# Optimization experiments

Hardware: AMD Instinct MI355X
Metric: run time of the kernel (lower is better)

## Reference

```python
import jax, jax.numpy as jnp
import numpy as np

N_LAYERS = 8
LAYER_NAMES = ['self', 'cross'] * 4
D_MODEL = 256
NHEAD = 8
HEAD_DIM = D_MODEL // NHEAD
EPS_ATTN = 1e-6
EPS_LN = 1e-5


def _xavier(key, shape):
    fan_in, fan_out = shape[-2], shape[-1]
    limit = float(np.sqrt(6.0 / (fan_in + fan_out)))
    return jax.random.uniform(key, shape, jnp.float32, -limit, limit)


def setup_inputs() -> dict:
    key = jax.random.key(0)
    ks = jax.random.split(key, 9)
    B, L, C = 4, 4800, D_MODEL
    inp = {
        'feat0': jax.random.normal(ks[0], (B, L, C), jnp.float32),
        'feat1': jax.random.normal(ks[1], (B, L, C), jnp.float32),
        # stacked per-layer params (layers are deepcopies, independently init'd)
        'Wq': _xavier(ks[2], (N_LAYERS, C, C)),
        'Wk': _xavier(ks[3], (N_LAYERS, C, C)),
        'Wv': _xavier(ks[4], (N_LAYERS, C, C)),
        'Wm': _xavier(ks[5], (N_LAYERS, C, C)),
        'W1': _xavier(ks[6], (N_LAYERS, 2 * C, 2 * C)),
        'W2': _xavier(ks[7], (N_LAYERS, 2 * C, C)),
        'ln1_w': jnp.ones((N_LAYERS, C), jnp.float32),
        'ln1_b': jnp.zeros((N_LAYERS, C), jnp.float32),
        'ln2_w': jnp.ones((N_LAYERS, C), jnp.float32),
        'ln2_b': jnp.zeros((N_LAYERS, C), jnp.float32),
    }
    return inp


def _layernorm(x, w, b):
    mu = jnp.mean(x, axis=-1, keepdims=True)
    var = jnp.mean(jnp.square(x - mu), axis=-1, keepdims=True)
    return (x - mu) * jax.lax.rsqrt(var + EPS_LN) * w + b


def _encoder_layer(x, source, Wq, Wk, Wv, Wm, W1, W2, ln1_w, ln1_b, ln2_w, ln2_b):
    bs, L, C = x.shape
    S = source.shape[1]
    q = (x @ Wq).reshape(bs, L, NHEAD, HEAD_DIM)
    k = (source @ Wk).reshape(bs, S, NHEAD, HEAD_DIM)
    v = (source @ Wv).reshape(bs, S, NHEAD, HEAD_DIM)
    # linear (kernelized) attention: phi(x) = elu(x) + 1
    Q = jax.nn.elu(q) + 1.0
    K = jax.nn.elu(k) + 1.0
    v_len = S
    v_scaled = v / v_len
    KV = jnp.einsum('nshd,nshv->nhdv', K, v_scaled)          # [N,H,D,D]
    Z = 1.0 / (jnp.einsum('nlhd,nhd->nlh', Q, K.sum(axis=1)) + EPS_ATTN)
    msg = jnp.einsum('nlhd,nhdv,nlh->nlhv', Q, KV, Z) * v_len  # [N,L,H,D]
    msg = msg.reshape(bs, L, C) @ Wm
    msg = _layernorm(msg, ln1_w, ln1_b)
    h = jnp.concatenate([x, msg], axis=-1)                   # [N,L,2C]
    h = jnp.maximum(h @ W1, 0.0) @ W2
    h = _layernorm(h, ln2_w, ln2_b)
    return x + h


def reference(feat0, feat1, Wq, Wk, Wv, Wm, W1, W2, ln1_w, ln1_b, ln2_w, ln2_b):
    for i, name in enumerate(LAYER_NAMES):
        p = (Wq[i], Wk[i], Wv[i], Wm[i], W1[i], W2[i],
             ln1_w[i], ln1_b[i], ln2_w[i], ln2_b[i])
        if name == 'self':
            feat0 = _encoder_layer(feat0, feat0, *p)
            feat1 = _encoder_layer(feat1, feat1, *p)
        else:  # cross
            feat0 = _encoder_layer(feat0, feat1, *p)
            feat1 = _encoder_layer(feat1, feat0, *p)
    return (feat0, feat1)
```

## Files before the change

kernel.cpp:

```cpp
#include <hip/hip_runtime.h>

typedef __attribute__((ext_vector_type(8))) short short8;
typedef __attribute__((ext_vector_type(4))) float f32x4;

#define DEV static __device__ __forceinline__

DEV unsigned short f2bf(float x) {
  union { float f; unsigned int u; } c; c.f = x;
  unsigned int r = c.u + 0x7fffu + ((c.u >> 16) & 1u);
  return (unsigned short)(r >> 16);
}
DEV float bf2f(unsigned short s) {
  union { unsigned int u; float f; } c; c.u = ((unsigned int)s) << 16;
  return c.f;
}
DEV float elu1(float x) { return x > 0.f ? x + 1.f : __expf(x); }

DEV void gload_lds16(const void* g, void* l) {
  __builtin_amdgcn_global_load_lds(
      (const __attribute__((address_space(1))) unsigned int*)g,
      (__attribute__((address_space(3))) unsigned int*)l, 16, 0, 0);
}

__global__ __launch_bounds__(256)
void wprep(const float* __restrict__ src, unsigned short* __restrict__ dst,
           int K, int N, int dls) {
  const int layer = blockIdx.z;
  src += (size_t)layer * K * N;
  dst += (size_t)layer * dls;
  __shared__ float tile[64][65];
  const int n0 = blockIdx.x * 64, k0 = blockIdx.y * 64;
  const int c = threadIdx.x & 63, r4 = threadIdx.x >> 6;
#pragma unroll
  for (int i = 0; i < 16; ++i) {
    int r = (i << 2) + r4;
    tile[r][c] = src[(size_t)(k0 + r) * N + n0 + c];
  }
  __syncthreads();
#pragma unroll
  for (int i = 0; i < 16; ++i) {
    int r = (i << 2) + r4;
    dst[(size_t)(n0 + r) * K + k0 + c] = f2bf(tile[c][r]);
  }
}

__global__ __launch_bounds__(256)
void init_feat(const float* __restrict__ src, float* __restrict__ dstf,
               unsigned short* __restrict__ dstb, int n4) {
  int i = blockIdx.x * 256 + threadIdx.x;
  if (i >= n4) return;
  float4 v = ((const float4*)src)[i];
  ((float4*)dstf)[i] = v;
  ushort4 o;
  o.x = f2bf(v.x); o.y = f2bf(v.y); o.z = f2bf(v.z); o.w = f2bf(v.w);
  ((ushort4*)dstb)[i] = o;
}

template<int EPI>
__global__ __launch_bounds__(256)
void gemm_bt(const unsigned short* __restrict__ A0,
             const unsigned short* __restrict__ A1,
             const unsigned short* __restrict__ BT,
             unsigned short* __restrict__ Cb, unsigned short* __restrict__ Cb2,
             int M, int N, int K, int lda) {
  __shared__ __align__(16) unsigned short smem[16896];
  unsigned short* As = smem;
  unsigned short* Bs = smem + 8192;
  const int tid = threadIdx.x;
  const int lane = tid & 63, wave = tid >> 6;
  const int tn = N >> 7;
  const int bm = (int)blockIdx.x / tn, bn = (int)blockIdx.x % tn;
  const int wm = (wave >> 1) << 6, wn = (wave & 1) << 6;
  const int lr = lane & 15, lk = lane >> 4;

  f32x4 acc[4][4];
#pragma unroll
  for (int i = 0; i < 4; ++i)
#pragma unroll
    for (int j = 0; j < 4; ++j) acc[i][j] = (f32x4){0.f, 0.f, 0.f, 0.f};

  for (int k0 = 0; k0 < K; k0 += 64) {
#pragma unroll
    for (int i = 0; i < 4; ++i) {
      const int cb = (i << 2) + wave;
      const int id = (cb << 6) + lane;
      const int row = id >> 3, ck = id & 7;
      const int gk = k0 + ((ck ^ (row & 7)) << 3);
      const unsigned short* srcA;
      if (A1) {
        srcA = (gk < 256) ? (A0 + (size_t)(bm * 128 + row) * 256 + gk)
                          : (A1 + (size_t)(bm * 128 + row) * 256 + (gk - 256));
      } else {
        srcA = A0 + (size_t)(bm * 128 + row) * lda + gk;
      }
      gload_lds16(srcA, As + (size_t)cb * 512);
      const unsigned short* srcB = BT + (size_t)(bn * 128 + row) * K + gk;
      gload_lds16(srcB, Bs + (size_t)cb * 512);
    }
    __syncthreads();
#pragma unroll
    for (int kk = 0; kk < 2; ++kk) {
      short8 af[4], bfr[4];
#pragma unroll
      for (int mi = 0; mi < 4; ++mi) {
        const int row = wm + mi * 16 + lr;
        const int ck = ((kk << 2) + lk) ^ (row & 7);
        af[mi] = *(const short8*)(As + row * 64 + ck * 8);
      }
#pragma unroll
      for (int ni = 0; ni < 4; ++ni) {
        const int row = wn + ni * 16 + lr;
        const int ck = ((kk << 2) + lk) ^ (row & 7);
        bfr[ni] = *(const short8*)(Bs + row * 64 + ck * 8);
      }
#pragma unroll
      for (int mi = 0; mi < 4; ++mi)
#pragma unroll
        for (int ni = 0; ni < 4; ++ni)
          acc[mi][ni] = __builtin_amdgcn_mfma_f32_16x16x32_bf16(af[mi], bfr[ni], acc[mi][ni], 0, 0, 0);
    }
    __syncthreads();
  }

  unsigned short* dst;
  int cstride, colofs, act;
  if (EPI == 1)      { dst = Cb;  cstride = N;   colofs = bn * 128; act = 1; }
  else if (EPI == 2) { dst = Cb;  cstride = 512; colofs = bn * 128; act = (bn < 2) ? 2 : 0; }
  else if (EPI == 3) { dst = Cb;  cstride = 256; colofs = bn * 128; act = 2; }
  else {
    if (bn < 2) { dst = Cb;  cstride = 256; colofs = bn * 128;       act = 2; }
    else        { dst = Cb2; cstride = 512; colofs = bn * 128 - 256; act = (bn < 4) ? 2 : 0; }
  }

  unsigned short* Ct = smem;
  const int cr = lk << 2;
#pragma unroll
  for (int mi = 0; mi < 4; ++mi)
#pragma unroll
    for (int ni = 0; ni < 4; ++ni)
#pragma unroll
      for (int j = 0; j < 4; ++j) {
        float v = acc[mi][ni][j];
        v = (act == 1) ? fmaxf(v, 0.f) : (act == 2) ? elu1(v) : v;
        Ct[(wm + mi * 16 + cr + j) * 132 + (wn + ni * 16 + lr)] = f2bf(v);
      }
  __syncthreads();
  const int rr = lane >> 4, cc8 = (lane & 15) << 3;
#pragma unroll
  for (int s = 0; s < 8; ++s) {
    const int rl = (wave << 5) + (s << 2) + rr;
    uint2 lo = *(const uint2*)(Ct + rl * 132 + cc8);
    uint2 hi = *(const uint2*)(Ct + rl * 132 + cc8 + 4);
    uint4 val = make_uint4(lo.x, lo.y, hi.x, hi.y);
    *(uint4*)(dst + (size_t)(bm * 128 + rl) * cstride + colofs + cc8) = val;
  }
}

template<int EPI>
__global__ __launch_bounds__(512)
void gemm_ln(const unsigned short* __restrict__ A, const unsigned short* __restrict__ BT,
             const float* __restrict__ lnw, const float* __restrict__ lnb,
             const float* __restrict__ xres, float* __restrict__ outf,
             unsigned short* __restrict__ outb, int K) {
  __shared__ __align__(16) unsigned short smem[24576];
  unsigned short* As = smem;
  unsigned short* Bs = smem + 8192;
  const int tid = threadIdx.x;
  const int lane = tid & 63, wid = tid >> 6;
  const int bm = blockIdx.x;
  const int wm = (wid >> 2) << 6, wn = (wid & 3) << 6;
  const int lr = lane & 15, lk = lane >> 4;

  f32x4 acc[4][4];
#pragma unroll
  for (int i = 0; i < 4; ++i)
#pragma unroll
    for (int j = 0; j < 4; ++j) acc[i][j] = (f32x4){0.f, 0.f, 0.f, 0.f};

  for (int k0 = 0; k0 < K; k0 += 64) {
#pragma unroll
    for (int i = 0; i < 2; ++i) {
      const int cb = i * 8 + wid;
      const int id = (cb << 6) + lane;
      const int row = id >> 3, ck = id & 7;
      const int gk = k0 + ((ck ^ (row & 7)) << 3);
      gload_lds16(A + (size_t)(bm * 128 + row) * K + gk, As + (size_t)cb * 512);
    }
#pragma unroll
    for (int i = 0; i < 4; ++i) {
      const int cb = i * 8 + wid;
      const int id = (cb << 6) + lane;
      const int row = id >> 3, ck = id & 7;
      const int gk = k0 + ((ck ^ (row & 7)) << 3);
      gload_lds16(BT + (size_t)row * K + gk, Bs + (size_t)cb * 512);
    }
    __syncthreads();
#pragma unroll
    for (int kk = 0; kk < 2; ++kk) {
      short8 af[4], bfr[4];
#pragma unroll
      for (int mi = 0; mi < 4; ++mi) {
        const int row = wm + mi * 16 + lr;
        const int ck = ((kk << 2) + lk) ^ (row & 7);
        af[mi] = *(const short8*)(As + row * 64 + ck * 8);
      }
#pragma unroll
      for (int ni = 0; ni < 4; ++ni) {
        const int row = wn + ni * 16 + lr;
        const int ck = ((kk << 2) + lk) ^ (row & 7);
        bfr[ni] = *(const short8*)(Bs + row * 64 + ck * 8);
      }
#pragma unroll
      for (int mi = 0; mi < 4; ++mi)
#pragma unroll
        for (int ni = 0; ni < 4; ++ni)
          acc[mi][ni] = __builtin_amdgcn_mfma_f32_16x16x32_bf16(af[mi], bfr[ni], acc[mi][ni], 0, 0, 0);
    }
    __syncthreads();
  }

  float* red = (float*)smem;
  const int cr = lk << 2;
  float wv[4], bv[4];
#pragma unroll
  for (int ni = 0; ni < 4; ++ni) {
    wv[ni] = lnw[wn + ni * 16 + lr];
    bv[ni] = lnb[wn + ni * 16 + lr];
  }
#pragma unroll
  for (int mi = 0; mi < 4; ++mi) {
#pragma unroll
    for (int j = 0; j < 4; ++j) {
      float s = 0.f, q = 0.f;
#pragma unroll
      for (int ni = 0; ni < 4; ++ni) {
        float v = acc[mi][ni][j];
        s += v; q += v * v;
      }
#pragma unroll
      for (int o = 1; o < 16; o <<= 1) {
        s += __shfl_xor(s, o);
        q += __shfl_xor(q, o);
      }
      if (lr == 0) {
        int row = wm + mi * 16 + cr + j;
        red[row * 8 + (wid & 3) * 2] = s;
        red[row * 8 + (wid & 3) * 2 + 1] = q;
      }
    }
  }
  __syncthreads();

  unsigned short* Pt = smem + 2048;
#pragma unroll
  for (int th = 0; th < 2; ++th) {
    if ((wm >> 6) == th) {
#pragma unroll
      for (int mi = 0; mi < 4; ++mi) {
#pragma unroll
        for (int j = 0; j < 4; ++j) {
          const int lrow = mi * 16 + cr + j;
          const int row = wm + lrow;
          const size_t grow = (size_t)bm * 128 + row;
          float s = red[row * 8] + red[row * 8 + 2] + red[row * 8 + 4] + red[row * 8 + 6];
          float q = red[row * 8 + 1] + red[row * 8 + 3] + red[row * 8 + 5] + red[row * 8 + 7];
          float mu = s * (1.f / 256.f);
          float var = q * (1.f / 256.f) - mu * mu;
          float rstd = rsqrtf(var + 1e-5f);
#pragma unroll
          for (int ni = 0; ni < 4; ++ni) {
            int col = wn + ni * 16 + lr;
            float y = (acc[mi][ni][j] - mu) * rstd * wv[ni] + bv[ni];
            if (EPI == 0) {
              Pt[lrow * 264 + col] = f2bf(y);
            } else {
              float o = xres[grow * 256 + col] + y;
              outf[grow * 256 + col] = o;
              Pt[lrow * 264 + col] = f2bf(o);
            }
          }
        }
      }
    }
    __syncthreads();
#pragma unroll
    for (int s = 0; s < 4; ++s) {
      const int qid = wid * 256 + lane * 4 + s;
      const int row = qid >> 5, colq = (qid & 31) << 3;
      uint2 lo = *(const uint2*)(Pt + row * 264 + colq);
      uint2 hi = *(const uint2*)(Pt + row * 264 + colq + 4);
      uint4 val = make_uint4(lo.x, lo.y, hi.x, hi.y);
      *(uint4*)(outb + (size_t)(bm * 128 + th * 64 + row) * 256 + colq) = val;
    }
    __syncthreads();
  }
}

__global__ __launch_bounds__(256)
void kv_partial(const unsigned short* __restrict__ kvb, float* __restrict__ part) {
  const int ch = blockIdx.x, h = blockIdx.y, n = blockIdx.z;
  const int t = threadIdx.x, wave = t >> 6, lane = t & 63;
  __shared__ float kb[4][8][36];
  __shared__ float vb[4][8][36];
  const int dq = lane >> 3, vq = lane & 7;
  float a[4][4];
  float ks[4] = {0.f, 0.f, 0.f, 0.f};
#pragma unroll
  for (int i = 0; i < 4; ++i)
#pragma unroll
    for (int j = 0; j < 4; ++j) a[i][j] = 0.f;

  const int s_base = ch * 480 + wave * 120;
  const int half = lane >> 5, l = lane & 31, r = l >> 2, c8 = l & 3;
  const unsigned short* src = kvb + ((size_t)n * 4800 + s_base + r) * 512 +
                              half * 256 + h * 32 + c8 * 8;
  float* dst = (half ? &vb[wave][r][0] : &kb[wave][r][0]) + c8 * 8;

  for (int it = 0; it < 15; ++it) {
    __syncthreads();
    short8 raw = *(const short8*)(src + (size_t)it * 8 * 512);
#pragma unroll
    for (int e = 0; e < 8; ++e) dst[e] = bf2f((unsigned short)raw[e]);
    __syncthreads();
#pragma unroll
    for (int si = 0; si < 8; ++si) {
      float4 kq = *(const float4*)&kb[wave][si][dq * 4];
      float4 vv = *(const float4*)&vb[wave][si][vq * 4];
      ks[0] += kq.x; ks[1] += kq.y; ks[2] += kq.z; ks[3] += kq.w;
      a[0][0] += kq.x * vv.x; a[0][1] += kq.x * vv.y; a[0][2] += kq.x * vv.z; a[0][3] += kq.x * vv.w;
      a[1][0] += kq.y * vv.x; a[1][1] += kq.y * vv.y; a[1][2] += kq.y * vv.z; a[1][3] += kq.y * vv.w;
      a[2][0] += kq.z * vv.x; a[2][1] += kq.z * vv.y; a[2][2] += kq.z * vv.z; a[2][3] += kq.z * vv.w;
      a[3][0] += kq.w * vv.x; a[3][1] += kq.w * vv.y; a[3][2] += kq.w * vv.z; a[3][3] += kq.w * vv.w;
    }
  }
  float* pb = part + ((size_t)((n * 8 + h) * 40 + ch * 4 + wave)) * 1056;
#pragma unroll
  for (int i = 0; i < 4; ++i) {
#pragma unroll
    for (int j = 0; j < 4; ++j) pb[(dq * 4 + i) * 32 + vq * 4 + j] = a[i][j];
    if (vq == 0) pb[1024 + dq * 4 + i] = ks[i];
  }
}

__global__ __launch_bounds__(256)
void kv_reduce(const float* __restrict__ part, unsigned short* __restrict__ KVb,
               float* __restrict__ Ksum) {
  const int nh = blockIdx.x, t = threadIdx.x;
  const float* pb = part + (size_t)nh * 40 * 1056;
#pragma unroll
  for (int j = 0; j < 4; ++j) {
    int e = t * 4 + j;
    float s = 0.f;
    for (int c = 0; c < 40; ++c) s += pb[c * 1056 + e];
    int dd = e >> 5, vv = e & 31;
    size_t addr = ((size_t)(nh * 2 + (vv >> 4)) * 64 + ((dd >> 3) * 16 + (vv & 15))) * 8 + (dd & 7);
    KVb[addr] = f2bf(s);
  }
  if (t < 32) {
    float s = 0.f;
    for (int c = 0; c < 40; ++c) s += pb[c * 1056 + 1024 + t];
    Ksum[nh * 32 + t] = s;
  }
}

__global__ __launch_bounds__(256)
void msg_kernel(const unsigned short* __restrict__ qb, const unsigned short* __restrict__ KVb,
                const float* __restrict__ Ksum, unsigned short* __restrict__ msg, int qoff) {
  const int n = blockIdx.y;
  const int wave = threadIdx.x >> 6, lane = threadIdx.x & 63;
  const int lr = lane & 15, lk = lane >> 4;
  const int lrow = blockIdx.x * 64 + wave * 16 + lr;
  const unsigned short* qrow = qb + ((size_t)qoff + (size_t)n * 4800 + lrow) * 256;
  const short8* kvv = (const short8*)KVb;
  for (int h = 0; h < 8; ++h) {
    short8 af = *(const short8*)(qrow + h * 32 + lk * 8);
    const float* ksp = Ksum + (n * 8 + h) * 32 + lk * 8;
    float zp = 0.f;
#pragma unroll
    for (int j = 0; j < 8; ++j) zp += bf2f((unsigned short)af[j]) * ksp[j];
    zp += __shfl_xor(zp, 16);
    zp += __shfl_xor(zp, 32);
    float z = 1.f / (zp + 1e-6f);
    short8 b0 = kvv[((size_t)(n * 8 + h) * 2 + 0) * 64 + lane];
    short8 b1 = kvv[((size_t)(n * 8 + h) * 2 + 1) * 64 + lane];
    f32x4 acc0 = (f32x4){0.f, 0.f, 0.f, 0.f}, acc1 = (f32x4){0.f, 0.f, 0.f, 0.f};
    acc0 = __builtin_amdgcn_mfma_f32_16x16x32_bf16(af, b0, acc0, 0, 0, 0);
    acc1 = __builtin_amdgcn_mfma_f32_16x16x32_bf16(af, b1, acc1, 0, 0, 0);
#pragma unroll
    for (int j = 0; j < 4; ++j) {
      int rr = lk * 4 + j;
      float zj = __shfl(z, rr);
      int row = blockIdx.x * 64 + wave * 16 + rr;
      size_t base = ((size_t)n * 4800 + row) * 256 + h * 32;
      msg[base + lr] = f2bf(acc0[j] * zj);
      msg[base + 16 + lr] = f2bf(acc1[j] * zj);
    }
  }
}

extern "C" void kernel_launch(void* const* d_in, const int* in_sizes, int n_in,
                              void* d_out, int out_size, void* d_ws, size_t ws_size,
                              hipStream_t stream) {
  (void)in_sizes; (void)n_in; (void)out_size; (void)ws_size;
  const float* feat0 = (const float*)d_in[0];
  const float* feat1 = (const float*)d_in[1];
  const float* Wq = (const float*)d_in[2];
  const float* Wk = (const float*)d_in[3];
  const float* Wv = (const float*)d_in[4];
  const float* Wm = (const float*)d_in[5];
  const float* W1 = (const float*)d_in[6];
  const float* W2 = (const float*)d_in[7];
  const float* ln1w = (const float*)d_in[8];
  const float* ln1b = (const float*)d_in[9];
  const float* ln2w = (const float*)d_in[10];
  const float* ln2b = (const float*)d_in[11];

  float* F0 = (float*)d_out;
  float* F1 = F0 + (size_t)4915200;

  size_t off = 0;
  auto alloc = [&](size_t bytes) -> void* {
    void* p = (char*)d_ws + off;
    off += (bytes + 255) & ~(size_t)255;
    return p;
  };
  unsigned short* Fb     = (unsigned short*)alloc((size_t)38400 * 256 * 2);
  unsigned short* qb     = (unsigned short*)alloc((size_t)38400 * 256 * 2);
  unsigned short* kvb    = (unsigned short*)alloc((size_t)38400 * 512 * 2);
  unsigned short* msgb   = (unsigned short*)alloc((size_t)38400 * 256 * 2);
  unsigned short* msglnb = (unsigned short*)alloc((size_t)38400 * 256 * 2);
  float*          part   = (float*)alloc((size_t)64 * 40 * 1056 * 4);
  unsigned short* KVb    = (unsigned short*)alloc((size_t)65536 * 2);
  float*          Ksum   = (float*)alloc((size_t)2048 * 4);
  unsigned short* WqkvT  = (unsigned short*)alloc((size_t)8 * 196608 * 2);
  unsigned short* WmT    = (unsigned short*)alloc((size_t)8 * 65536 * 2);
  unsigned short* W1T    = (unsigned short*)alloc((size_t)8 * 262144 * 2);
  unsigned short* W2T    = (unsigned short*)alloc((size_t)8 * 131072 * 2);
  unsigned short* h1b = kvb;
  unsigned short* F0b = Fb;
  unsigned short* F1b = Fb + (size_t)19200 * 256;

  init_feat<<<4800, 256, 0, stream>>>(feat0, F0, F0b, 1228800);
  init_feat<<<4800, 256, 0, stream>>>(feat1, F1, F1b, 1228800);

  wprep<<<dim3(4, 4, 8), 256, 0, stream>>>(Wq, WqkvT, 256, 256, 196608);
  wprep<<<dim3(4, 4, 8), 256, 0, stream>>>(Wk, WqkvT + 65536, 256, 256, 196608);
  wprep<<<dim3(4, 4, 8), 256, 0, stream>>>(Wv, WqkvT + 131072, 256, 256, 196608);
  wprep<<<dim3(4, 4, 8), 256, 0, stream>>>(Wm, WmT, 256, 256, 65536);
  wprep<<<dim3(8, 8, 8), 256, 0, stream>>>(W1, W1T, 512, 512, 262144);
  wprep<<<dim3(4, 8, 8), 256, 0, stream>>>(W2, W2T, 512, 256, 131072);

  auto ffn = [&](unsigned short* Xb, float* X, int M, int i) {
    const int g128 = M >> 7;
    gemm_ln<0><<<g128, 512, 0, stream>>>(msgb, WmT + (size_t)i * 65536,
                                         ln1w + i * 256, ln1b + i * 256,
                                         nullptr, nullptr, msglnb, 256);
    gemm_bt<1><<<g128 * 4, 256, 0, stream>>>(Xb, msglnb, W1T + (size_t)i * 262144,
                                             h1b, nullptr, M, 512, 512, 256);
    gemm_ln<1><<<g128, 512, 0, stream>>>(h1b, W2T + (size_t)i * 131072,
                                         ln2w + i * 256, ln2b + i * 256,
                                         X, X, Xb, 512);
  };

  for (int i = 0; i < 8; ++i) {
    if ((i & 1) == 0) {
      gemm_bt<4><<<1800, 256, 0, stream>>>(Fb, nullptr, WqkvT + (size_t)i * 196608,
                                           qb, kvb, 38400, 768, 256, 256);
      kv_partial<<<dim3(10, 8, 8), 256, 0, stream>>>(kvb, part);
      kv_reduce<<<64, 256, 0, stream>>>(part, KVb, Ksum);
      msg_kernel<<<dim3(75, 8), 256, 0, stream>>>(qb, KVb, Ksum, msgb, 0);
      ffn(Fb, F0, 38400, i);
    } else {
      gemm_bt<3><<<600, 256, 0, stream>>>(Fb, nullptr, WqkvT + (size_t)i * 196608,
                                          qb, nullptr, 38400, 256, 256, 256);
      gemm_bt<2><<<600, 256, 0, stream>>>(F1b, nullptr, WqkvT + (size_t)i * 196608 + 65536,
                                          kvb, nullptr, 19200, 512, 256, 256);
      kv_partial<<<dim3(10, 8, 4), 256, 0, stream>>>(kvb, part);
      kv_reduce<<<32, 256, 0, stream>>>(part, KVb, Ksum);
      msg_kernel<<<dim3(75, 4), 256, 0, stream>>>(qb, KVb, Ksum, msgb, 0);
      ffn(F0b, F0, 19200, i);
      gemm_bt<2><<<600, 256, 0, stream>>>(F0b, nullptr, WqkvT + (size_t)i * 196608 + 65536,
                                          kvb, nullptr, 19200, 512, 256, 256);
      kv_partial<<<dim3(10, 8, 4), 256, 0, stream>>>(kvb, part);
      kv_reduce<<<32, 256, 0, stream>>>(part, KVb, Ksum);
      msg_kernel<<<dim3(75, 4), 256, 0, stream>>>(qb, KVb, Ksum, msgb, 19200);
      ffn(F1b, F1, 19200, i);
    }
  }
}
```

Measured before the change: 1.681 ms.

## Double-buffer LDS tiles in both GEMM kernels to overlap loads with MFMA

Both GEMM kernels now keep two LDS buffers and issue the global-to-LDS loads for the next K tile before computing on the current one. Partial vmcnt waits plus raw barriers replace the full __syncthreads, so that memory latency overlaps with MFMA work. This doubles LDS use per block (64KB and 96KB), which may lower occupancy. The hand-written vmcnt counts must match the number of outstanding loads per thread, or tiles could be read before they arrive.

```diff
diff --git a/kernel.cpp b/kernel.cpp
--- a/kernel.cpp
+++ b/kernel.cpp
@@ -63,9 +63,9 @@
              const unsigned short* __restrict__ BT,
              unsigned short* __restrict__ Cb, unsigned short* __restrict__ Cb2,
              int M, int N, int K, int lda) {
-  __shared__ __align__(16) unsigned short smem[16896];
+  __shared__ __align__(16) unsigned short smem[32768];
   unsigned short* As = smem;
-  unsigned short* Bs = smem + 8192;
+  unsigned short* Bs = smem + 16384;
   const int tid = threadIdx.x;
   const int lane = tid & 63, wave = tid >> 6;
   const int tn = N >> 7;
@@ -79,7 +79,7 @@
 #pragma unroll
     for (int j = 0; j < 4; ++j) acc[i][j] = (f32x4){0.f, 0.f, 0.f, 0.f};
 
-  for (int k0 = 0; k0 < K; k0 += 64) {
+  auto stageAB = [&](int nb, int k0) {
 #pragma unroll
     for (int i = 0; i < 4; ++i) {
       const int cb = (i << 2) + wave;
@@ -93,11 +93,26 @@
       } else {
         srcA = A0 + (size_t)(bm * 128 + row) * lda + gk;
       }
-      gload_lds16(srcA, As + (size_t)cb * 512);
+      gload_lds16(srcA, As + nb * 8192 + (size_t)cb * 512);
       const unsigned short* srcB = BT + (size_t)(bn * 128 + row) * K + gk;
-      gload_lds16(srcB, Bs + (size_t)cb * 512);
-    }
-    __syncthreads();
+      gload_lds16(srcB, Bs + nb * 8192 + (size_t)cb * 512);
+    }
+  };
+
+  const int nt = K >> 6;
+  stageAB(0, 0);
+  for (int t = 0; t < nt; ++t) {
+    const int cur = t & 1;
+    if (t + 1 < nt) {
+      stageAB(cur ^ 1, (t + 1) << 6);
+      asm volatile("s_waitcnt vmcnt(8)" ::: "memory");
+    } else {
+      asm volatile("s_waitcnt vmcnt(0)" ::: "memory");
+    }
+    __builtin_amdgcn_s_barrier();
+    __builtin_amdgcn_sched_barrier(0);
+    const unsigned short* Ac = As + cur * 8192;
+    const unsigned short* Bc = Bs + cur * 8192;
 #pragma unroll
     for (int kk = 0; kk < 2; ++kk) {
       short8 af[4], bfr[4];
@@ -105,13 +120,13 @@
       for (int mi = 0; mi < 4; ++mi) {
         const int row = wm + mi * 16 + lr;
         const int ck = ((kk << 2) + lk) ^ (row & 7);
-        af[mi] = *(const short8*)(As + row * 64 + ck * 8);
+        af[mi] = *(const short8*)(Ac + row * 64 + ck * 8);
       }
 #pragma unroll
       for (int ni = 0; ni < 4; ++ni) {
         const int row = wn + ni * 16 + lr;
         const int ck = ((kk << 2) + lk) ^ (row & 7);
-        bfr[ni] = *(const short8*)(Bs + row * 64 + ck * 8);
+        bfr[ni] = *(const short8*)(Bc + row * 64 + ck * 8);
       }
 #pragma unroll
       for (int mi = 0; mi < 4; ++mi)
@@ -119,7 +134,8 @@
         for (int ni = 0; ni < 4; ++ni)
           acc[mi][ni] = __builtin_amdgcn_mfma_f32_16x16x32_bf16(af[mi], bfr[ni], acc[mi][ni], 0, 0, 0);
     }
-    __syncthreads();
+    __builtin_amdgcn_s_barrier();
+    __builtin_amdgcn_sched_barrier(0);
   }
 
   unsigned short* dst;
@@ -162,9 +178,9 @@
              const float* __restrict__ lnw, const float* __restrict__ lnb,
              const float* __restrict__ xres, float* __restrict__ outf,
              unsigned short* __restrict__ outb, int K) {
-  __shared__ __align__(16) unsigned short smem[24576];
+  __shared__ __align__(16) unsigned short smem[49152];
   unsigned short* As = smem;
-  unsigned short* Bs = smem + 8192;
+  unsigned short* Bs = smem + 16384;
   const int tid = threadIdx.x;
   const int lane = tid & 63, wid = tid >> 6;
   const int bm = blockIdx.x;
@@ -177,14 +193,14 @@
 #pragma unroll
     for (int j = 0; j < 4; ++j) acc[i][j] = (f32x4){0.f, 0.f, 0.f, 0.f};
 
-  for (int k0 = 0; k0 < K; k0 += 64) {
+  auto stageAB = [&](int nb, int k0) {
 #pragma unroll
     for (int i = 0; i < 2; ++i) {
       const int cb = i * 8 + wid;
       const int id = (cb << 6) + lane;
       const int row = id >> 3, ck = id & 7;
       const int gk = k0 + ((ck ^ (row & 7)) << 3);
-      gload_lds16(A + (size_t)(bm * 128 + row) * K + gk, As + (size_t)cb * 512);
+      gload_lds16(A + (size_t)(bm * 128 + row) * K + gk, As + nb * 8192 + (size_t)cb * 512);
     }
 #pragma unroll
     for (int i = 0; i < 4; ++i) {
@@ -192,9 +208,24 @@
       const int id = (cb << 6) + lane;
       const int row = id >> 3, ck = id & 7;
       const int gk = k0 + ((ck ^ (row & 7)) << 3);
-      gload_lds16(BT + (size_t)row * K + gk, Bs + (size_t)cb * 512);
-    }
-    __syncthreads();
+      gload_lds16(BT + (size_t)row * K + gk, Bs + nb * 16384 + (size_t)cb * 512);
+    }
+  };
+
+  const int nt = K >> 6;
+  stageAB(0, 0);
+  for (int t = 0; t < nt; ++t) {
+    const int cur = t & 1;
+    if (t + 1 < nt) {
+      stageAB(cur ^ 1, (t + 1) << 6);
+      asm volatile("s_waitcnt vmcnt(6)" ::: "memory");
+    } else {
+      asm volatile("s_waitcnt vmcnt(0)" ::: "memory");
+    }
+    __builtin_amdgcn_s_barrier();
+    __builtin_amdgcn_sched_barrier(0);
+    const unsigned short* Ac = As + cur * 8192;
+    const unsigned short* Bc = Bs + cur * 16384;
 #pragma unroll
     for (int kk = 0; kk < 2; ++kk) {
       short8 af[4], bfr[4];
@@ -202,13 +233,13 @@
       for (int mi = 0; mi < 4; ++mi) {
         const int row = wm + mi * 16 + lr;
         const int ck = ((kk << 2) + lk) ^ (row & 7);
-        af[mi] = *(const short8*)(As + row * 64 + ck * 8);
+        af[mi] = *(const short8*)(Ac + row * 64 + ck * 8);
       }
 #pragma unroll
       for (int ni = 0; ni < 4; ++ni) {
         const int row = wn + ni * 16 + lr;
         const int ck = ((kk << 2) + lk) ^ (row & 7);
-        bfr[ni] = *(const short8*)(Bs + row * 64 + ck * 8);
+        bfr[ni] = *(const short8*)(Bc + row * 64 + ck * 8);
       }
 #pragma unroll
       for (int mi = 0; mi < 4; ++mi)
@@ -216,7 +247,8 @@
         for (int ni = 0; ni < 4; ++ni)
           acc[mi][ni] = __builtin_amdgcn_mfma_f32_16x16x32_bf16(af[mi], bfr[ni], acc[mi][ni], 0, 0, 0);
     }
-    __syncthreads();
+    __builtin_amdgcn_s_barrier();
+    __builtin_amdgcn_sched_barrier(0);
   }
 
   float* red = (float*)smem;
```

Measured after the change: 1.731 ms. 1.03x slower.

## Restructure kv_partial to load full KV rows via direct global-to-LDS copies

Applied to the files above, without the earlier changes.

kv_partial now assigns each block a chunk of 120 rows across all 8 heads, with each wave handling two heads, instead of one head per block with waves splitting rows. Each step copies whole 8-row slabs of the bf16 K|V buffer into LDS with global_load_lds and converts to float at compute time. This replaces narrow per-head strided global reads and per-element LDS float stores with contiguous row loads. In exchange each thread holds twice the accumulators, and the grid shrinks from 640 to 320 blocks, which lowers parallelism.

```diff
diff --git a/kernel.cpp b/kernel.cpp
--- a/kernel.cpp
+++ b/kernel.cpp
@@ -298,47 +298,60 @@
 
 __global__ __launch_bounds__(256)
 void kv_partial(const unsigned short* __restrict__ kvb, float* __restrict__ part) {
-  const int ch = blockIdx.x, h = blockIdx.y, n = blockIdx.z;
-  const int t = threadIdx.x, wave = t >> 6, lane = t & 63;
-  __shared__ float kb[4][8][36];
-  __shared__ float vb[4][8][36];
+  const int ch = blockIdx.x, n = blockIdx.y;
+  const int tid = threadIdx.x, wid = tid >> 6, lane = tid & 63;
+  __shared__ __align__(16) unsigned short kvs[8 * 512];
   const int dq = lane >> 3, vq = lane & 7;
-  float a[4][4];
-  float ks[4] = {0.f, 0.f, 0.f, 0.f};
-#pragma unroll
-  for (int i = 0; i < 4; ++i)
-#pragma unroll
-    for (int j = 0; j < 4; ++j) a[i][j] = 0.f;
-
-  const int s_base = ch * 480 + wave * 120;
-  const int half = lane >> 5, l = lane & 31, r = l >> 2, c8 = l & 3;
-  const unsigned short* src = kvb + ((size_t)n * 4800 + s_base + r) * 512 +
-                              half * 256 + h * 32 + c8 * 8;
-  float* dst = (half ? &vb[wave][r][0] : &kb[wave][r][0]) + c8 * 8;
+  float a[2][4][4];
+  float ks[2][4];
+#pragma unroll
+  for (int hh = 0; hh < 2; ++hh) {
+#pragma unroll
+    for (int i = 0; i < 4; ++i) {
+      ks[hh][i] = 0.f;
+#pragma unroll
+      for (int j = 0; j < 4; ++j) a[hh][i][j] = 0.f;
+    }
+  }
+  const int r0 = ch * 120;
+  const size_t rowbase = (size_t)n * 4800 + r0;
 
   for (int it = 0; it < 15; ++it) {
     __syncthreads();
-    short8 raw = *(const short8*)(src + (size_t)it * 8 * 512);
-#pragma unroll
-    for (int e = 0; e < 8; ++e) dst[e] = bf2f((unsigned short)raw[e]);
-    __syncthreads();
-#pragma unroll
-    for (int si = 0; si < 8; ++si) {
-      float4 kq = *(const float4*)&kb[wave][si][dq * 4];
-      float4 vv = *(const float4*)&vb[wave][si][vq * 4];
-      ks[0] += kq.x; ks[1] += kq.y; ks[2] += kq.z; ks[3] += kq.w;
-      a[0][0] += kq.x * vv.x; a[0][1] += kq.x * vv.y; a[0][2] += kq.x * vv.z; a[0][3] += kq.x * vv.w;
-      a[1][0] += kq.y * vv.x; a[1][1] += kq.y * vv.y; a[1][2] += kq.y * vv.z; a[1][3] += kq.y * vv.w;
-      a[2][0] += kq.z * vv.x; a[2][1] += kq.z * vv.y; a[2][2] += kq.z * vv.z; a[2][3] += kq.z * vv.w;
-      a[3][0] += kq.w * vv.x; a[3][1] += kq.w * vv.y; a[3][2] += kq.w * vv.z; a[3][3] += kq.w * vv.w;
-    }
-  }
-  float* pb = part + ((size_t)((n * 8 + h) * 40 + ch * 4 + wave)) * 1056;
-#pragma unroll
-  for (int i = 0; i < 4; ++i) {
-#pragma unroll
-    for (int j = 0; j < 4; ++j) pb[(dq * 4 + i) * 32 + vq * 4 + j] = a[i][j];
-    if (vq == 0) pb[1024 + dq * 4 + i] = ks[i];
+#pragma unroll
+    for (int i = 0; i < 2; ++i) {
+      const int c = (i << 8) + tid;
+      const int row = c >> 6, col8 = (c & 63) << 3;
+      gload_lds16(kvb + (rowbase + it * 8 + row) * 512 + col8, kvs + (size_t)c * 8);
+    }
+    __syncthreads();
+#pragma unroll
+    for (int s = 0; s < 8; ++s) {
+#pragma unroll
+      for (int hh = 0; hh < 2; ++hh) {
+        const int h = wid * 2 + hh;
+        ushort4 kr = *(const ushort4*)(kvs + s * 512 + h * 32 + dq * 4);
+        ushort4 vr = *(const ushort4*)(kvs + s * 512 + 256 + h * 32 + vq * 4);
+        float k0 = bf2f(kr.x), k1 = bf2f(kr.y), k2 = bf2f(kr.z), k3 = bf2f(kr.w);
+        float v0 = bf2f(vr.x), v1 = bf2f(vr.y), v2 = bf2f(vr.z), v3 = bf2f(vr.w);
+        ks[hh][0] += k0; ks[hh][1] += k1; ks[hh][2] += k2; ks[hh][3] += k3;
+        a[hh][0][0] += k0 * v0; a[hh][0][1] += k0 * v1; a[hh][0][2] += k0 * v2; a[hh][0][3] += k0 * v3;
+        a[hh][1][0] += k1 * v0; a[hh][1][1] += k1 * v1; a[hh][1][2] += k1 * v2; a[hh][1][3] += k1 * v3;
+        a[hh][2][0] += k2 * v0; a[hh][2][1] += k2 * v1; a[hh][2][2] += k2 * v2; a[hh][2][3] += k2 * v3;
+        a[hh][3][0] += k3 * v0; a[hh][3][1] += k3 * v1; a[hh][3][2] += k3 * v2; a[hh][3][3] += k3 * v3;
+      }
+    }
+  }
+#pragma unroll
+  for (int hh = 0; hh < 2; ++hh) {
+    const int h = wid * 2 + hh;
+    float* pb = part + ((size_t)((n * 8 + h) * 40 + ch)) * 1056;
+#pragma unroll
+    for (int i = 0; i < 4; ++i) {
+#pragma unroll
+      for (int j = 0; j < 4; ++j) pb[(dq * 4 + i) * 32 + vq * 4 + j] = a[hh][i][j];
+      if (vq == 0) pb[1024 + dq * 4 + i] = ks[hh][i];
+    }
   }
 }
 
@@ -466,7 +479,7 @@
     if ((i & 1) == 0) {
       gemm_bt<4><<<1800, 256, 0, stream>>>(Fb, nullptr, WqkvT + (size_t)i * 196608,
                                            qb, kvb, 38400, 768, 256, 256);
-      kv_partial<<<dim3(10, 8, 8), 256, 0, stream>>>(kvb, part);
+      kv_partial<<<dim3(40, 8), 256, 0, stream>>>(kvb, part);
       kv_reduce<<<64, 256, 0, stream>>>(part, KVb, Ksum);
       msg_kernel<<<dim3(75, 8), 256, 0, stream>>>(qb, KVb, Ksum, msgb, 0);
       ffn(Fb, F0, 38400, i);
@@ -475,13 +488,13 @@
                                           qb, nullptr, 38400, 256, 256, 256);
       gemm_bt<2><<<600, 256, 0, stream>>>(F1b, nullptr, WqkvT + (size_t)i * 196608 + 65536,
                                           kvb, nullptr, 19200, 512, 256, 256);
-      kv_partial<<<dim3(10, 8, 4), 256, 0, stream>>>(kvb, part);
+      kv_partial<<<dim3(40, 4), 256, 0, stream>>>(kvb, part);
       kv_reduce<<<32, 256, 0, stream>>>(part, KVb, Ksum);
       msg_kernel<<<dim3(75, 4), 256, 0, stream>>>(qb, KVb, Ksum, msgb, 0);
       ffn(F0b, F0, 19200, i);
       gemm_bt<2><<<600, 256, 0, stream>>>(F0b, nullptr, WqkvT + (size_t)i * 196608 + 65536,
                                           kvb, nullptr, 19200, 512, 256, 256);
-      kv_partial<<<dim3(10, 8, 4), 256, 0, stream>>>(kvb, part);
+      kv_partial<<<dim3(40, 4), 256, 0, stream>>>(kvb, part);
       kv_reduce<<<32, 256, 0, stream>>>(part, KVb, Ksum);
       msg_kernel<<<dim3(75, 4), 256, 0, stream>>>(qb, KVb, Ksum, msgb, 19200);
       ffn(F1b, F1, 19200, i);
```

After: 1.757 ms. 4.5% more time.
